# Optimization experiments

Hardware: AMD Instinct MI355X
Metric: run time of the kernel (lower is better)

The kernel has to match this reference:

```python
import jax, jax.numpy as jnp
import numpy as np

N_LAYER = 6
EPS = 1e-5
THETA = 2.0 ** 16


def _ln(x):
    # LayerNorm without affine params, eps=1e-5 (torch default)
    m = x.mean(-1, keepdims=True)
    v = ((x - m) ** 2).mean(-1, keepdims=True)
    return (x - m) * jax.lax.rsqrt(v + EPS)


def _rope(phases, v):
    # rotate-half over interleaved pairs, phases are in cycles (mod 1 -> radians)
    v_rot = jnp.stack([-v[..., 1::2], v[..., ::2]], axis=-1).reshape(v.shape)
    ph = (phases % 1.0) * (2.0 * jnp.pi)
    return v * jnp.cos(ph) + v_rot * jnp.sin(ph)


def _forward(x, conv_w, conv_b, pos_embed, encoder, encoder_v, decoder, freqs, head_w, head_b):
    B, Cin, H, W = x.shape
    nh, D, N = encoder.shape
    P = conv_w.shape[-1]
    hp, wp = H // P, W // P
    T = hp * wp
    # patch embed: Conv2d(k=P, s=P) == unfold + matmul
    xp = x.reshape(B, Cin, hp, P, wp, P)
    tokens = jnp.einsum('bchpwq,dcpq->bhwd', xp, conv_w).reshape(B, T, D) + conv_b
    h = tokens + pos_embed  # (B, T, D); the unit head dim is handled by einsum broadcasting
    phases = jnp.arange(T, dtype=jnp.float32).reshape(1, 1, T, 1) * freqs  # (1,1,T,N)
    scale = 1.0 / jnp.sqrt(jnp.asarray(N, dtype=x.dtype))
    for _ in range(N_LAYER):  # weights are SHARED across layers, as in the module
        hn = _ln(h)  # (B, T, D)
        x_sparse = jax.nn.relu(jnp.einsum('btd,hdn->bhtn', hn, encoder))  # (B,nh,T,N)
        qr = _rope(phases, x_sparse)
        scores = jax.nn.softmax(jnp.einsum('bhtn,bhsn->bhts', qr, qr) * scale, axis=-1)
        yKV = _ln(jnp.einsum('bhts,bsd->bhtd', scores, hn))  # V = ln'd x, broadcast over heads
        y_sparse = jax.nn.relu(jnp.einsum('bhtd,hdn->bhtn', yKV, encoder_v))
        xy_sparse = x_sparse * y_sparse  # (B,nh,T,N)
        z = xy_sparse.transpose(0, 2, 1, 3).reshape(B, T, nh * N)  # (B,T,nh*N), head-major flatten
        yMLP = _ln(z @ decoder)  # (B,T,D)
        h = _ln(hn + yMLP)
    pooled = _ln(h.mean(axis=1))  # (B,D)
    return pooled @ head_w.T + head_b


def setup_inputs():
    key = jax.random.key(0)
    B, Cin, H, P = 64, 3, 224, 16
    D, nh, mult, ncls = 768, 12, 8, 1000
    N = mult * D // nh  # 512
    T = (H // P) ** 2  # 196
    ks = jax.random.split(key, 7)

    def xav(k, shape, fan_in, fan_out):
        a = (6.0 / (fan_in + fan_out)) ** 0.5
        return jax.random.uniform(k, shape, jnp.float32, -a, a)

    x = jax.random.normal(ks[0], (B, Cin, H, H), jnp.float32)
    conv_w = xav(ks[1], (D, Cin, P, P), Cin * P * P, D)
    conv_b = jnp.zeros((D,), jnp.float32)
    pos_embed = jax.random.normal(ks[2], (1, T, D), jnp.float32) * 0.02
    encoder = xav(ks[3], (nh, D, N), D, N)
    encoder_v = xav(ks[4], (nh, D, N), D, N)
    decoder = xav(ks[5], (nh * N, D), nh * N, D)
    i = jnp.arange(N, dtype=jnp.float32)
    freqs = ((1.0 / THETA) ** ((i // 2) * 2.0 / N)).reshape(1, 1, 1, N)  # paired RoPE freqs
    head_w = xav(ks[6], (ncls, D), D, ncls)
    head_b = jnp.zeros((ncls,), jnp.float32)
    return dict(x=x, conv_w=conv_w, conv_b=conv_b, pos_embed=pos_embed,
                encoder=encoder, encoder_v=encoder_v, decoder=decoder,
                freqs=freqs, head_w=head_w, head_b=head_b)


def reference(x, conv_w, conv_b, pos_embed, encoder, encoder_v, decoder, freqs, head_w, head_b):
    return _forward(x, conv_w, conv_b, pos_embed, encoder, encoder_v, decoder, freqs, head_w, head_b)
```

## Files before the change

kernel.cpp:

```cpp
#include <hip/hip_runtime.h>
#include <hip/hip_bf16.h>


typedef short bf16x8 __attribute__((ext_vector_type(8)));
typedef float f32x4 __attribute__((ext_vector_type(4)));
typedef unsigned short u16;

#define LN_EPS 1e-5f
#define SM_SCALE 0.044194173824159216f
#define TWO_PI 6.283185307179586f
#define MC 3136

typedef __attribute__((address_space(3))) unsigned char* as3p;
typedef const __attribute__((address_space(1))) unsigned char* as1p;

__device__ __forceinline__ void gload16(const u16* g, u16* l) {
    __builtin_amdgcn_global_load_lds((as1p)(const void*)g, (as3p)(void*)l, 16, 0, 0);
}

__device__ __forceinline__ u16 f2bf(float f) {
    __hip_bfloat16 h = __float2bfloat16(f);
    return *reinterpret_cast<u16*>(&h);
}
__device__ __forceinline__ float bf2f(u16 u) {
    return __uint_as_float(((unsigned)u) << 16);
}

__device__ __forceinline__ float block_reduce_sum(float v, float* sm) {
    #pragma unroll
    for (int o = 32; o; o >>= 1) v += __shfl_xor(v, o);
    if ((threadIdx.x & 63) == 0) sm[threadIdx.x >> 6] = v;
    __syncthreads();
    float r = sm[0] + sm[1] + sm[2] + sm[3];
    __syncthreads();
    return r;
}

__device__ __forceinline__ void gemm_core64(const u16* __restrict__ A, int lda,
                                            const u16* __restrict__ Bt, int ldb,
                                            int ksteps, f32x4 acc[4][4],
                                            u16* lds_a, u16* lds_b) {
    const int tid = threadIdx.x;
    const int lane = tid & 63;
    const int wave = tid >> 6;
    const int wr = (wave >> 1) * 64;
    const int wc = (wave & 1) * 64;
    const int lr = lane & 15;
    const int lg = lane >> 4;
    const int rx = lr & 7;
    const int srow = tid >> 3;
    const int gslot = (tid & 7) ^ (srow & 7);
    const u16* ga = A + (long)srow * lda + gslot * 8;
    const u16* gb = Bt + (long)srow * ldb + gslot * 8;
    u16* la = lds_a + tid * 8;
    u16* lb = lds_b + tid * 8;
    for (int k0 = 0; k0 < ksteps; ++k0) {
        __syncthreads();
        #pragma unroll
        for (int j = 0; j < 4; ++j) {
            gload16(ga + (long)(j * 32) * lda, la + j * 2048);
            gload16(gb + (long)(j * 32) * ldb, lb + j * 2048);
        }
        ga += 64; gb += 64;
        __syncthreads();
        bf16x8 af[2][4], bfr[2][4];
        #pragma unroll
        for (int kk = 0; kk < 2; ++kk) {
            const int ps = ((lg + kk * 4) ^ rx) * 8;
            #pragma unroll
            for (int m = 0; m < 4; m++)
                af[kk][m] = *(const bf16x8*)&lds_a[(wr + 16 * m + lr) * 64 + ps];
            #pragma unroll
            for (int n = 0; n < 4; n++)
                bfr[kk][n] = *(const bf16x8*)&lds_b[(wc + 16 * n + lr) * 64 + ps];
        }
        #pragma unroll
        for (int kk = 0; kk < 2; ++kk)
            #pragma unroll
            for (int m = 0; m < 4; m++)
                #pragma unroll
                for (int n = 0; n < 4; n++)
                    acc[m][n] = __builtin_amdgcn_mfma_f32_16x16x32_bf16(
                        af[kk][m], bfr[kk][n], acc[m][n], 0, 0, 0);
    }
}

#define GEMM64_PROLOGUE                                 \
    __shared__ alignas(16) u16 lds_ab[2 * 128 * 64];    \
    u16* lds_a = lds_ab;                                \
    u16* lds_b = lds_ab + 128 * 64;                     \
    f32x4 acc[4][4];                                    \
    _Pragma("unroll")                                   \
    for (int m = 0; m < 4; m++)                         \
        _Pragma("unroll")                               \
        for (int n = 0; n < 4; n++)                     \
            acc[m][n] = (f32x4){0.f, 0.f, 0.f, 0.f};

#define EPI_VARS                                        \
    const int lane = threadIdx.x & 63;                  \
    const int wave = threadIdx.x >> 6;                  \
    const int ewr = (wave >> 1) * 64 + (lane >> 4) * 4; \
    const int ewc = (wave & 1) * 64 + (lane & 15);

__global__ __launch_bounds__(256) void k_pack_patches(const float* __restrict__ x,
                                                      u16* __restrict__ ap) {
    int idx = blockIdx.x * 256 + threadIdx.x;
    int r = idx / 768, k = idx - r * 768;
    int b = r / 196, t = r - b * 196;
    int hp = t / 14, wp = t - hp * 14;
    int c = k >> 8, rem = k & 255, p = rem >> 4, q = rem & 15;
    long src = ((long)(b * 3 + c) * 224 + hp * 16 + p) * 224 + wp * 16 + q;
    ap[idx] = f2bf(x[src]);
}

__global__ __launch_bounds__(256) void k_cast(const float* __restrict__ s,
                                              u16* __restrict__ d, int n) {
    int i = blockIdx.x * 256 + threadIdx.x;
    if (i < n) d[i] = f2bf(s[i]);
}

__global__ __launch_bounds__(256) void k_transpose_cast(const float* __restrict__ src,
                                                        u16* __restrict__ dst,
                                                        int R, int C) {
    __shared__ float tile[32][33];
    int c0 = blockIdx.x * 32, r0 = blockIdx.y * 32;
    long base = (long)blockIdx.z * R * C;
    int i = threadIdx.x >> 5, j = threadIdx.x & 31;
    #pragma unroll
    for (int p = 0; p < 4; p++) {
        int rr = i + p * 8;
        tile[rr][j] = src[base + (long)(r0 + rr) * C + c0 + j];
    }
    __syncthreads();
    #pragma unroll
    for (int p = 0; p < 4; p++) {
        int rr = i + p * 8;
        dst[base + (long)(c0 + rr) * R + r0 + j] = f2bf(tile[j][rr]);
    }
}

__global__ __launch_bounds__(256) void k_rope_tab(const float* __restrict__ freqs,
                                                  float* __restrict__ tc,
                                                  float* __restrict__ ts) {
    int idx = blockIdx.x * 256 + threadIdx.x;
    int t = idx >> 9, n = idx & 511;
    float ph = (float)t * freqs[n];
    ph = (ph - floorf(ph)) * TWO_PI;
    tc[idx] = cosf(ph);
    ts[idx] = sinf(ph);
}

__global__ __launch_bounds__(256) void k_colsum(const float* __restrict__ encv,
                                                float* __restrict__ cs) {
    int h = blockIdx.y, c = blockIdx.x * 256 + threadIdx.x;
    const float* base = encv + (long)h * 768 * 512 + c;
    float a = 0.f;
    for (int d = 0; d < 768; d++) a += base[(long)d * 512];
    cs[h * 512 + c] = a;
}

__global__ __launch_bounds__(256) void k_gemm_tokens(const u16* __restrict__ ap,
                                                     const u16* __restrict__ bw,
                                                     const float* __restrict__ cb,
                                                     const float* __restrict__ pe,
                                                     float* __restrict__ hout) {
    GEMM64_PROLOGUE
    int row0 = blockIdx.x * 128, col0 = blockIdx.y * 128;
    gemm_core64(ap + (long)row0 * 768, 768, bw + (long)col0 * 768, 768, 12, acc, lds_a, lds_b);
    EPI_VARS
    const int tid = threadIdx.x;
    float* TF = (float*)lds_ab;
    #pragma unroll
    for (int hf = 0; hf < 2; ++hf) {
        __syncthreads();
        if ((ewr >> 6) == hf) {
            #pragma unroll
            for (int m = 0; m < 4; m++)
                #pragma unroll
                for (int n = 0; n < 4; n++)
                    #pragma unroll
                    for (int i = 0; i < 4; i++) {
                        int row = row0 + ewr + 16 * m + i;
                        int col = col0 + ewc + 16 * n;
                        int t = row % 196;
                        TF[(ewr - hf * 64 + 16 * m + i) * 128 + ewc + 16 * n] =
                            acc[m][n][i] + cb[col] + pe[t * 768 + col];
                    }
        }
        __syncthreads();
        #pragma unroll
        for (int q = 0; q < 8; ++q) {
            int chunk = tid + q * 256;
            int r = chunk >> 5, c = chunk & 31;
            *(f32x4*)&hout[(long)(row0 + hf * 64 + r) * 768 + col0 + c * 4] =
                *(f32x4*)&TF[r * 128 + c * 4];
        }
    }
}

__global__ __launch_bounds__(256) void k_gemm_xs(const u16* __restrict__ hnb,
                                                 const u16* __restrict__ enct,
                                                 const float* __restrict__ tc,
                                                 const float* __restrict__ tsn,
                                                 u16* __restrict__ xs,
                                                 u16* __restrict__ qr) {
    GEMM64_PROLOGUE
    int p = blockIdx.x + 25 * blockIdx.y;
    int w = (p & 7) * 150 + (p >> 3);
    int row0 = (w % 25) * 128, col0 = (w / 25) * 128;
    int head = col0 >> 9, nn0 = col0 & 511;
    gemm_core64(hnb + (long)row0 * 768, 768,
                enct + ((long)head * 512 + nn0) * 768, 768, 12, acc, lds_a, lds_b);
    EPI_VARS
    const int tid = threadIdx.x;
    u16* TU = lds_ab;
    __syncthreads();
    #pragma unroll
    for (int m = 0; m < 4; m++)
        #pragma unroll
        for (int n = 0; n < 4; n++)
            #pragma unroll
            for (int i = 0; i < 4; i++)
                TU[(ewr + 16 * m + i) * 128 + ewc + 16 * n] =
                    f2bf(fmaxf(acc[m][n][i], 0.f));
    __syncthreads();
    #pragma unroll
    for (int q = 0; q < 8; ++q) {
        int chunk = tid + q * 256;
        int r = chunk >> 4, c = chunk & 15;
        int row = row0 + r;
        if (row < MC)
            *(bf16x8*)&xs[((long)head * MC + row) * 512 + nn0 + c * 8] =
                *(bf16x8*)&TU[r * 128 + c * 8];
    }
    #pragma unroll
    for (int q = 0; q < 8; ++q) {
        int chunk = tid + q * 256;
        int r = chunk >> 4, c = chunk & 15;
        int row = row0 + r;
        if (row < MC) {
            int t = row % 196;
            int nn = nn0 + c * 8;
            bf16x8 v8 = *(bf16x8*)&TU[r * 128 + c * 8];
            f32x4 cs0 = *(const f32x4*)&tc[t * 512 + nn];
            f32x4 cs1 = *(const f32x4*)&tc[t * 512 + nn + 4];
            f32x4 sn0 = *(const f32x4*)&tsn[t * 512 + nn];
            f32x4 sn1 = *(const f32x4*)&tsn[t * 512 + nn + 4];
            float v[8], qv[8];
            #pragma unroll
            for (int j = 0; j < 8; j++) v[j] = bf2f((u16)v8[j]);
            #pragma unroll
            for (int j = 0; j < 2; j++) {
                qv[2 * j]     = v[2 * j] * cs0[2 * j]     - v[2 * j + 1] * sn0[2 * j];
                qv[2 * j + 1] = v[2 * j + 1] * cs0[2 * j + 1] + v[2 * j] * sn0[2 * j + 1];
                qv[4 + 2 * j]     = v[4 + 2 * j] * cs1[2 * j]     - v[4 + 2 * j + 1] * sn1[2 * j];
                qv[4 + 2 * j + 1] = v[4 + 2 * j + 1] * cs1[2 * j + 1] + v[4 + 2 * j] * sn1[2 * j + 1];
            }
            bf16x8 o8;
            #pragma unroll
            for (int j = 0; j < 8; j++) o8[j] = (short)f2bf(qv[j]);
            *(bf16x8*)&qr[((long)head * MC + row) * 512 + nn] = o8;
        }
    }
}

__global__ __launch_bounds__(256) void k_attn(const u16* __restrict__ qr,
                                              const u16* __restrict__ hnT,
                                              u16* __restrict__ ykv,
                                              float* __restrict__ stats) {
    __shared__ alignas(16) u16 Pl[128 * 232];
    __shared__ alignas(16) u16 Bl[128 * 64];
    __shared__ float part[2][128][2];
    const int tid = threadIdx.x, lane = tid & 63, wave = tid >> 6;
    const int wr = (wave >> 1) * 64, wc = (wave & 1) * 64;
    const int lr = lane & 15, lg = lane >> 4, lk = lg * 8;
    const int rx = lr & 7;
    const int p = blockIdx.x;
    const int xcd = p & 7, slot = p >> 3;
    const int bL = 2 * xcd + (slot >= 24);
    const int sub = (slot >= 24) ? slot - 24 : slot;
    const int h = sub >> 1, rt = sub & 1;
    const int bh = h * 16 + bL;
    const int row0 = rt * 128;
    const u16* qbase = qr + (long)bh * 196 * 512;

    f32x4 acc0[4][4], acc1[4][4];
    #pragma unroll
    for (int m = 0; m < 4; m++)
        #pragma unroll
        for (int n = 0; n < 4; n++) {
            acc0[m][n] = (f32x4){0.f, 0.f, 0.f, 0.f};
            acc1[m][n] = (f32x4){0.f, 0.f, 0.f, 0.f};
        }
    {
        u16* sA = Pl;
        u16* sB = Pl + 128 * 64;
        gemm_core64(qbase + (long)row0 * 512, 512, qbase, 512, 8, acc0, sA, sB);
        gemm_core64(qbase + (long)row0 * 512, 512, qbase + 128 * 512, 512, 8, acc1, sA, sB);
    }

    const int rb = wr + (lane >> 4) * 4;
    #pragma unroll
    for (int m = 0; m < 4; m++)
        #pragma unroll
        for (int i = 0; i < 4; i++) {
            float mx = -1e30f;
            #pragma unroll
            for (int n = 0; n < 4; n++) {
                int c0 = wc + 16 * n + lr;
                if (c0 < 196) mx = fmaxf(mx, acc0[m][n][i]);
                if (c0 + 128 < 196) mx = fmaxf(mx, acc1[m][n][i]);
            }
            #pragma unroll
            for (int o = 1; o < 16; o <<= 1) mx = fmaxf(mx, __shfl_xor(mx, o));
            if (lr == 0) part[0][rb + 16 * m + i][wave & 1] = mx;
        }
    __syncthreads();
    #pragma unroll
    for (int m = 0; m < 4; m++)
        #pragma unroll
        for (int i = 0; i < 4; i++) {
            int row = rb + 16 * m + i;
            float rmx = fmaxf(part[0][row][0], part[0][row][1]);
            float s = 0.f;
            #pragma unroll
            for (int n = 0; n < 4; n++) {
                int c0 = wc + 16 * n + lr;
                float e0 = (c0 < 196) ? __expf((acc0[m][n][i] - rmx) * SM_SCALE) : 0.f;
                float e1 = (c0 + 128 < 196) ? __expf((acc1[m][n][i] - rmx) * SM_SCALE) : 0.f;
                acc0[m][n][i] = e0; acc1[m][n][i] = e1;
                s += e0 + e1;
            }
            #pragma unroll
            for (int o = 1; o < 16; o <<= 1) s += __shfl_xor(s, o);
            if (lr == 0) part[1][row][wave & 1] = s;
        }
    __syncthreads();
    #pragma unroll
    for (int m = 0; m < 4; m++)
        #pragma unroll
        for (int i = 0; i < 4; i++) {
            int row = rb + 16 * m + i;
            float inv = 1.f / (part[1][row][0] + part[1][row][1]);
            #pragma unroll
            for (int n = 0; n < 4; n++) {
                int c0 = wc + 16 * n + lr;
                Pl[row * 232 + c0] = f2bf(acc0[m][n][i] * inv);
                if (c0 + 128 < 224)
                    Pl[row * 232 + c0 + 128] = f2bf(acc1[m][n][i] * inv);
            }
        }
    __syncthreads();
    { float* pf = &part[0][0][0]; pf[tid] = 0.f; pf[tid + 256] = 0.f; }
    __syncthreads();

    const int srow8 = tid >> 3;
    const int gsl8 = (tid & 7) ^ (srow8 & 7);
    const int srow2 = tid >> 2;
    const int gsl2 = (tid & 3) ^ ((srow2 >> 1) & 3);
    const int ps32 = (lg ^ ((lr >> 1) & 3)) * 8;
    const u16* hbase = hnT + (long)bL * 768 * 224;
    for (int cd = 0; cd < 6; ++cd) {
        const u16* Bt = hbase + (long)(cd * 128) * 224;
        f32x4 pacc[4][4];
        #pragma unroll
        for (int m = 0; m < 4; m++)
            #pragma unroll
            for (int n = 0; n < 4; n++) pacc[m][n] = (f32x4){0.f, 0.f, 0.f, 0.f};
        for (int k0 = 0; k0 < 3; ++k0) {
            __syncthreads();
            #pragma unroll
            for (int j = 0; j < 4; ++j)
                gload16(Bt + (long)(j * 32 + srow8) * 224 + k0 * 64 + gsl8 * 8,
                        Bl + j * 2048 + tid * 8);
            __syncthreads();
            bf16x8 af[2][4], bfr[2][4];
            #pragma unroll
            for (int kk = 0; kk < 2; ++kk) {
                const int ps = ((lg + 4 * kk) ^ rx) * 8;
                #pragma unroll
                for (int m = 0; m < 4; m++)
                    af[kk][m] = *(const bf16x8*)&Pl[(wr + 16 * m + lr) * 232 +
                                                    k0 * 64 + kk * 32 + lk];
                #pragma unroll
                for (int n = 0; n < 4; n++)
                    bfr[kk][n] = *(const bf16x8*)&Bl[(wc + 16 * n + lr) * 64 + ps];
            }
            #pragma unroll
            for (int kk = 0; kk < 2; ++kk)
                #pragma unroll
                for (int m = 0; m < 4; m++)
                    #pragma unroll
                    for (int n = 0; n < 4; n++)
                        pacc[m][n] = __builtin_amdgcn_mfma_f32_16x16x32_bf16(
                            af[kk][m], bfr[kk][n], pacc[m][n], 0, 0, 0);
        }
        {
            __syncthreads();
            gload16(Bt + (long)srow2 * 224 + 192 + gsl2 * 8, Bl + tid * 8);
            gload16(Bt + (long)(srow2 + 64) * 224 + 192 + gsl2 * 8, Bl + 2048 + tid * 8);
            __syncthreads();
            bf16x8 af[4], bfr[4];
            #pragma unroll
            for (int m = 0; m < 4; m++)
                af[m] = *(const bf16x8*)&Pl[(wr + 16 * m + lr) * 232 + 192 + lk];
            #pragma unroll
            for (int n = 0; n < 4; n++)
                bfr[n] = *(const bf16x8*)&Bl[(wc + 16 * n + lr) * 32 + ps32];
            #pragma unroll
            for (int m = 0; m < 4; m++)
                #pragma unroll
                for (int n = 0; n < 4; n++)
                    pacc[m][n] = __builtin_amdgcn_mfma_f32_16x16x32_bf16(
                        af[m], bfr[n], pacc[m][n], 0, 0, 0);
        }
        #pragma unroll
        for (int m = 0; m < 4; m++)
            #pragma unroll
            for (int i = 0; i < 4; i++) {
                float s = pacc[m][0][i] + pacc[m][1][i] + pacc[m][2][i] + pacc[m][3][i];
                float q2 = pacc[m][0][i] * pacc[m][0][i] + pacc[m][1][i] * pacc[m][1][i] +
                           pacc[m][2][i] * pacc[m][2][i] + pacc[m][3][i] * pacc[m][3][i];
                #pragma unroll
                for (int o = 1; o < 16; o <<= 1) {
                    s += __shfl_xor(s, o);
                    q2 += __shfl_xor(q2, o);
                }
                if (lr == 0) {
                    part[0][rb + 16 * m + i][wave & 1] += s;
                    part[1][rb + 16 * m + i][wave & 1] += q2;
                }
            }
        {
            const int ewr = wr + (lane >> 4) * 4;
            const int ewc = wc + lr;
            #pragma unroll
            for (int m = 0; m < 4; m++)
                #pragma unroll
                for (int n = 0; n < 4; n++)
                    #pragma unroll
                    for (int i = 0; i < 4; i++) {
                        int trow = row0 + ewr + 16 * m + i;
                        if (trow < 196)
                            ykv[((long)bh * 196 + trow) * 768 + cd * 128 + ewc + 16 * n] =
                                f2bf(pacc[m][n][i]);
                    }
        }
    }
    __syncthreads();
    if (tid < 128) {
        int trow = row0 + tid;
        if (trow < 196) {
            float s = part[0][tid][0] + part[0][tid][1];
            float q2 = part[1][tid][0] + part[1][tid][1];
            float mu = s * (1.f / 768.f);
            float var = q2 * (1.f / 768.f) - mu * mu;
            float2 st;
            st.x = mu;
            st.y = rsqrtf(var + LN_EPS);
            *(float2*)&stats[((long)bh * 196 + trow) * 2] = st;
        }
    }
}

__global__ __launch_bounds__(256) void k_gemm_ys(const u16* __restrict__ ykv,
                                                 const u16* __restrict__ encvt,
                                                 const u16* __restrict__ xs,
                                                 const float* __restrict__ stats,
                                                 const float* __restrict__ colsum,
                                                 u16* __restrict__ z) {
    GEMM64_PROLOGUE
    int p = blockIdx.x + 25 * (blockIdx.y + 4 * blockIdx.z);
    int w = (p & 7) * 150 + (p >> 3);
    int rt = w % 25, rem = w / 25;
    int ct = rem & 3, h = rem >> 2;
    int row0 = rt * 128, col0 = ct * 128;
    gemm_core64(ykv + ((long)h * MC + row0) * 768, 768,
                encvt + ((long)h * 512 + col0) * 768, 768, 12, acc, lds_a, lds_b);
    EPI_VARS
    const int tid = threadIdx.x;
    u16* TU = lds_ab;
    __syncthreads();
    #pragma unroll
    for (int q = 0; q < 8; ++q) {
        int chunk = tid + q * 256;
        int r = chunk >> 4, c = chunk & 15;
        *(bf16x8*)&TU[r * 128 + c * 8] =
            *(const bf16x8*)&xs[((long)h * MC + row0 + r) * 512 + col0 + c * 8];
    }
    __syncthreads();
    #pragma unroll
    for (int m = 0; m < 4; m++)
        #pragma unroll
        for (int i = 0; i < 4; i++) {
            int rloc = ewr + 16 * m + i;
            int row = row0 + rloc;
            float mu = 0.f, rs = 0.f;
            if (row < MC) {
                float2 st = *(const float2*)&stats[((long)h * MC + row) * 2];
                mu = st.x; rs = st.y;
            }
            #pragma unroll
            for (int n = 0; n < 4; n++) {
                int cloc = ewc + 16 * n;
                float cs = colsum[h * 512 + col0 + cloc];
                float v = (acc[m][n][i] - mu * cs) * rs;
                v = fmaxf(v, 0.f) * bf2f(TU[rloc * 128 + cloc]);
                TU[rloc * 128 + cloc] = f2bf(v);
            }
        }
    __syncthreads();
    #pragma unroll
    for (int q = 0; q < 8; ++q) {
        int chunk = tid + q * 256;
        int r = chunk >> 4, c = chunk & 15;
        int row = row0 + r;
        if (row < MC)
            *(bf16x8*)&z[(long)row * 6144 + h * 512 + col0 + c * 8] =
                *(bf16x8*)&TU[r * 128 + c * 8];
    }
}

__global__ __launch_bounds__(256) void k_gemm_mlp(const u16* __restrict__ z,
                                                  const u16* __restrict__ dect,
                                                  float* __restrict__ rawK) {
    GEMM64_PROLOGUE
    int p = blockIdx.x + 25 * (blockIdx.y + 6 * blockIdx.z);
    int w = (p & 7) * 75 + (p >> 3);
    int row0 = (w % 25) * 128, col0 = ((w / 25) % 6) * 128, s = w / 150;
    gemm_core64(z + (long)row0 * 6144 + s * 1536, 6144,
                dect + (long)col0 * 6144 + s * 1536, 6144, 24, acc, lds_a, lds_b);
    EPI_VARS
    const int tid = threadIdx.x;
    float* TF = (float*)lds_ab;
    float* raw = rawK + (long)s * MC * 768;
    #pragma unroll
    for (int hf = 0; hf < 2; ++hf) {
        __syncthreads();
        if ((ewr >> 6) == hf) {
            #pragma unroll
            for (int m = 0; m < 4; m++)
                #pragma unroll
                for (int n = 0; n < 4; n++)
                    #pragma unroll
                    for (int i = 0; i < 4; i++)
                        TF[(ewr - hf * 64 + 16 * m + i) * 128 + ewc + 16 * n] =
                            acc[m][n][i];
        }
        __syncthreads();
        #pragma unroll
        for (int q = 0; q < 8; ++q) {
            int chunk = tid + q * 256;
            int r = chunk >> 5, c = chunk & 31;
            int row = row0 + hf * 64 + r;
            if (row < MC)
                *(f32x4*)&raw[(long)row * 768 + col0 + c * 4] =
                    *(f32x4*)&TF[r * 128 + c * 4];
        }
    }
}

__global__ __launch_bounds__(256) void k_ln1(const float* __restrict__ h,
                                             u16* __restrict__ hnb) {
    __shared__ float sm[4];
    int r = blockIdx.x, tid = threadIdx.x;
    const float* p = h + (long)r * 768;
    float x0 = p[tid], x1 = p[tid + 256], x2 = p[tid + 512];
    float mean = block_reduce_sum(x0 + x1 + x2, sm) * (1.f / 768.f);
    float d0 = x0 - mean, d1 = x1 - mean, d2 = x2 - mean;
    float var = block_reduce_sum(d0 * d0 + d1 * d1 + d2 * d2, sm) * (1.f / 768.f);
    float rs = rsqrtf(var + LN_EPS);
    long ro = (long)r * 768;
    hnb[ro + tid] = f2bf(d0 * rs);
    hnb[ro + tid + 256] = f2bf(d1 * rs);
    hnb[ro + tid + 512] = f2bf(d2 * rs);
}

__global__ __launch_bounds__(256) void k_hnT(const u16* __restrict__ hnb,
                                             u16* __restrict__ hnT) {
    __shared__ u16 tile[32][33];
    int t0 = blockIdx.x * 32, d0 = blockIdx.y * 32, b = blockIdx.z;
    int i = threadIdx.x >> 5, j = threadIdx.x & 31;
    #pragma unroll
    for (int p = 0; p < 4; p++) {
        int t = t0 + i + p * 8;
        tile[i + p * 8][j] = (t < 196) ? hnb[((long)b * 196 + t) * 768 + d0 + j] : (u16)0;
    }
    __syncthreads();
    #pragma unroll
    for (int p = 0; p < 4; p++) {
        int dd = i + p * 8;
        hnT[((long)b * 768 + d0 + dd) * 224 + t0 + j] = tile[j][dd];
    }
}

__global__ __launch_bounds__(256) void k_final_h(const float* __restrict__ rawK,
                                                 u16* __restrict__ hnb) {
    __shared__ float sm[4];
    const long PS = (long)MC * 768;
    int r = blockIdx.x, tid = threadIdx.x;
    const float* rp = rawK + (long)r * 768;
    u16* hp = hnb + (long)r * 768;
    float y0 = rp[tid] + rp[tid + PS] + rp[tid + 2 * PS] + rp[tid + 3 * PS];
    float y1 = rp[tid + 256] + rp[tid + 256 + PS] + rp[tid + 256 + 2 * PS] + rp[tid + 256 + 3 * PS];
    float y2 = rp[tid + 512] + rp[tid + 512 + PS] + rp[tid + 512 + 2 * PS] + rp[tid + 512 + 3 * PS];
    float h0 = bf2f(hp[tid]), h1 = bf2f(hp[tid + 256]), h2 = bf2f(hp[tid + 512]);
    float mean = block_reduce_sum(y0 + y1 + y2, sm) * (1.f / 768.f);
    float d0 = y0 - mean, d1 = y1 - mean, d2 = y2 - mean;
    float var = block_reduce_sum(d0 * d0 + d1 * d1 + d2 * d2, sm) * (1.f / 768.f);
    float rs = rsqrtf(var + LN_EPS);
    float s0 = h0 + d0 * rs;
    float s1 = h1 + d1 * rs;
    float s2 = h2 + d2 * rs;
    mean = block_reduce_sum(s0 + s1 + s2, sm) * (1.f / 768.f);
    d0 = s0 - mean; d1 = s1 - mean; d2 = s2 - mean;
    var = block_reduce_sum(d0 * d0 + d1 * d1 + d2 * d2, sm) * (1.f / 768.f);
    rs = rsqrtf(var + LN_EPS);
    hp[tid] = f2bf(d0 * rs);
    hp[tid + 256] = f2bf(d1 * rs);
    hp[tid + 512] = f2bf(d2 * rs);
}

__global__ __launch_bounds__(256) void k_pool1(const u16* __restrict__ hnb,
                                               float* __restrict__ part) {
    int g = blockIdx.x, b = blockIdx.y, tid = threadIdx.x;
    const u16* base = hnb + ((long)b * 196 + g * 14) * 768;
    float a0 = 0.f, a1 = 0.f, a2 = 0.f;
    for (int t = 0; t < 14; t++) {
        const u16* p = base + (long)t * 768;
        a0 += bf2f(p[tid]); a1 += bf2f(p[tid + 256]); a2 += bf2f(p[tid + 512]);
    }
    float* pp = part + ((long)b * 14 + g) * 768;
    pp[tid] = a0; pp[tid + 256] = a1; pp[tid + 512] = a2;
}

__global__ __launch_bounds__(256) void k_pool2(const float* __restrict__ part,
                                               float* __restrict__ pooled) {
    __shared__ float sm[4];
    int b = blockIdx.x, tid = threadIdx.x;
    const float* pp = part + (long)b * 14 * 768;
    float a0 = 0.f, a1 = 0.f, a2 = 0.f;
    for (int g = 0; g < 14; g++) {
        a0 += pp[g * 768 + tid]; a1 += pp[g * 768 + tid + 256]; a2 += pp[g * 768 + tid + 512];
    }
    a0 *= (1.f / 196.f); a1 *= (1.f / 196.f); a2 *= (1.f / 196.f);
    float mean = block_reduce_sum(a0 + a1 + a2, sm) * (1.f / 768.f);
    float d0 = a0 - mean, d1 = a1 - mean, d2 = a2 - mean;
    float var = block_reduce_sum(d0 * d0 + d1 * d1 + d2 * d2, sm) * (1.f / 768.f);
    float rs = rsqrtf(var + LN_EPS);
    pooled[(long)b * 768 + tid] = d0 * rs;
    pooled[(long)b * 768 + tid + 256] = d1 * rs;
    pooled[(long)b * 768 + tid + 512] = d2 * rs;
}

__global__ __launch_bounds__(256) void k_head(const float* __restrict__ pooled,
                                              const float* __restrict__ hw,
                                              const float* __restrict__ hb,
                                              float* __restrict__ out) {
    __shared__ float pr[768];
    int b = blockIdx.y, tid = threadIdx.x;
    pr[tid] = pooled[(long)b * 768 + tid];
    pr[tid + 256] = pooled[(long)b * 768 + tid + 256];
    pr[tid + 512] = pooled[(long)b * 768 + tid + 512];
    __syncthreads();
    int c = blockIdx.x * 4 + (tid >> 6);
    int lane = tid & 63;
    const float* wrow = hw + (long)c * 768;
    float acc = 0.f;
    #pragma unroll
    for (int k = 0; k < 768; k += 64) acc += pr[k + lane] * wrow[k + lane];
    #pragma unroll
    for (int o = 32; o; o >>= 1) acc += __shfl_xor(acc, o);
    if (lane == 0) out[(long)b * 1000 + c] = acc + hb[c];
}

extern "C" void kernel_launch(void* const* d_in, const int* in_sizes, int n_in,
                              void* d_out, int out_size, void* d_ws, size_t ws_size,
                              hipStream_t stream) {
    const float* x     = (const float*)d_in[0];
    const float* convw = (const float*)d_in[1];
    const float* convb = (const float*)d_in[2];
    const float* pe    = (const float*)d_in[3];
    const float* enc   = (const float*)d_in[4];
    const float* encv  = (const float*)d_in[5];
    const float* dec   = (const float*)d_in[6];
    const float* freqs = (const float*)d_in[7];
    const float* hw    = (const float*)d_in[8];
    const float* hbias = (const float*)d_in[9];
    float* out = (float*)d_out;

    char* W = (char*)d_ws;
    size_t off = 0;
    auto ALLOC = [&](size_t bytes) {
        size_t o = off;
        off += (bytes + 255) & ~(size_t)255;
        return o;
    };
    float* bh    = (float*)(W + ALLOC(38535168));
    u16*   bhnb  = (u16*)  (W + ALLOC(19267584 + 524288));
    u16*   bhnT  = (u16*)  (W + ALLOC(22020096));
    u16*   benc  = (u16*)  (W + ALLOC(9437184));
    u16*   bencv = (u16*)  (W + ALLOC(9437184));
    u16*   bdec  = (u16*)  (W + ALLOC(9437184));
    float* btc   = (float*)(W + ALLOC(401408));
    float* bts   = (float*)(W + ALLOC(401408));
    float* bpool = (float*)(W + ALLOC(196608));
    float* bpart = (float*)(W + ALLOC(2752512));
    float* bstats= (float*)(W + ALLOC(301056));
    float* bcs   = (float*)(W + ALLOC(24576));
    char*  R1    = (char*) (W + ALLOC(38535168 + 2097152));
    char*  R2    = (char*) (W + ALLOC(57802752 + 524288));
    char*  R3    = (char*) (W + ALLOC(38535168 + 524288));
    (void)ws_size; (void)in_sizes; (void)n_in; (void)out_size;

    u16*   bap  = (u16*)R2;
    u16*   bcw  = (u16*)R3;
    u16*   qr   = (u16*)R1;
    u16*   z    = (u16*)R1;
    u16*   ykv  = (u16*)R2;
    float* rawK = (float*)R2;
    u16*   xs   = (u16*)R3;

    k_pack_patches<<<37632, 256, 0, stream>>>(x, bap);
    k_cast<<<2304, 256, 0, stream>>>(convw, bcw, 768 * 768);
    k_gemm_tokens<<<dim3(98, 6), 256, 0, stream>>>(bap, bcw, convb, pe, bh);
    k_transpose_cast<<<dim3(16, 24, 12), 256, 0, stream>>>(enc, benc, 768, 512);
    k_transpose_cast<<<dim3(16, 24, 12), 256, 0, stream>>>(encv, bencv, 768, 512);
    k_transpose_cast<<<dim3(24, 192, 1), 256, 0, stream>>>(dec, bdec, 6144, 768);
    k_rope_tab<<<392, 256, 0, stream>>>(freqs, btc, bts);
    k_colsum<<<dim3(2, 12), 256, 0, stream>>>(encv, bcs);
    k_ln1<<<12544, 256, 0, stream>>>(bh, bhnb);

    for (int L = 0; L < 6; ++L) {
        k_hnT<<<dim3(7, 24, 64), 256, 0, stream>>>(bhnb, bhnT);
        for (int c = 0; c < 4; ++c) {
            long r0 = (long)c * MC;
            k_gemm_xs<<<dim3(25, 48), 256, 0, stream>>>(
                bhnb + r0 * 768, benc, btc, bts, xs, qr);
            k_attn<<<384, 256, 0, stream>>>(
                qr, bhnT + (long)c * 16 * 768 * 224, ykv, bstats);
            k_gemm_ys<<<dim3(25, 4, 12), 256, 0, stream>>>(ykv, bencv, xs, bstats, bcs, z);
            k_gemm_mlp<<<dim3(25, 6, 4), 256, 0, stream>>>(z, bdec, rawK);
            k_final_h<<<MC, 256, 0, stream>>>(rawK, bhnb + r0 * 768);
        }
    }

    k_pool1<<<dim3(14, 64), 256, 0, stream>>>(bhnb, bpart);
    k_pool2<<<64, 256, 0, stream>>>(bpart, bpool);
    k_head<<<dim3(250, 64), 256, 0, stream>>>(bpool, hw, hbias, out);
}
```

Before: 5.914 ms.

## Split attention kernel into score/softmax and PV kernels via global probabilities

The fused attention kernel is split in two. The first computes QK^T and softmax and writes bf16 probabilities to a global scratch buffer, reusing the bh buffer, through a smaller LDS staging area. The second streams those probabilities back with global_load_lds tiles alongside hnT for the PV GEMM and LayerNorm stats. This cuts LDS use per kernel (no 128x232 P tile kept resident), which may allow more blocks per CU. The cost is an extra launch and a global round trip for P, and reusing bh as scratch assumes it is dead at that point.

```diff
diff --git a/kernel.cpp b/kernel.cpp
--- a/kernel.cpp
+++ b/kernel.cpp
@@ -102,6 +102,15 @@
     const int ewr = (wave >> 1) * 64 + (lane >> 4) * 4; \
     const int ewc = (wave & 1) * 64 + (lane & 15);
 
+#define ATTN_REMAP                                      \
+    const int p = blockIdx.x;                           \
+    const int xcd = p & 7, slot = p >> 3;               \
+    const int bL = 2 * xcd + (slot >= 24);              \
+    const int sub = (slot >= 24) ? slot - 24 : slot;    \
+    const int h = sub >> 1, rt = sub & 1;               \
+    const int bh = h * 16 + bL;                         \
+    const int row0 = rt * 128;
+
 __global__ __launch_bounds__(256) void k_pack_patches(const float* __restrict__ x,
                                                       u16* __restrict__ ap) {
     int idx = blockIdx.x * 256 + threadIdx.x;
@@ -264,24 +273,14 @@
     }
 }
 
-__global__ __launch_bounds__(256) void k_attn(const u16* __restrict__ qr,
-                                              const u16* __restrict__ hnT,
-                                              u16* __restrict__ ykv,
-                                              float* __restrict__ stats) {
-    __shared__ alignas(16) u16 Pl[128 * 232];
-    __shared__ alignas(16) u16 Bl[128 * 64];
+__global__ __launch_bounds__(256) void k_attn1(const u16* __restrict__ qr,
+                                               u16* __restrict__ Pg) {
+    __shared__ alignas(16) u16 sAB[2 * 128 * 64];
     __shared__ float part[2][128][2];
     const int tid = threadIdx.x, lane = tid & 63, wave = tid >> 6;
     const int wr = (wave >> 1) * 64, wc = (wave & 1) * 64;
-    const int lr = lane & 15, lg = lane >> 4, lk = lg * 8;
-    const int rx = lr & 7;
-    const int p = blockIdx.x;
-    const int xcd = p & 7, slot = p >> 3;
-    const int bL = 2 * xcd + (slot >= 24);
-    const int sub = (slot >= 24) ? slot - 24 : slot;
-    const int h = sub >> 1, rt = sub & 1;
-    const int bh = h * 16 + bL;
-    const int row0 = rt * 128;
+    const int lr = lane & 15;
+    ATTN_REMAP
     const u16* qbase = qr + (long)bh * 196 * 512;
 
     f32x4 acc0[4][4], acc1[4][4];
@@ -292,12 +291,10 @@
             acc0[m][n] = (f32x4){0.f, 0.f, 0.f, 0.f};
             acc1[m][n] = (f32x4){0.f, 0.f, 0.f, 0.f};
         }
-    {
-        u16* sA = Pl;
-        u16* sB = Pl + 128 * 64;
-        gemm_core64(qbase + (long)row0 * 512, 512, qbase, 512, 8, acc0, sA, sB);
-        gemm_core64(qbase + (long)row0 * 512, 512, qbase + 128 * 512, 512, 8, acc1, sA, sB);
-    }
+    gemm_core64(qbase + (long)row0 * 512, 512, qbase, 512, 8, acc0,
+                sAB, sAB + 128 * 64);
+    gemm_core64(qbase + (long)row0 * 512, 512, qbase + 128 * 512, 512, 8, acc1,
+                sAB, sAB + 128 * 64);
 
     const int rb = wr + (lane >> 4) * 4;
     #pragma unroll
@@ -336,30 +333,63 @@
             if (lr == 0) part[1][row][wave & 1] = s;
         }
     __syncthreads();
-    #pragma unroll
-    for (int m = 0; m < 4; m++)
-        #pragma unroll
-        for (int i = 0; i < 4; i++) {
-            int row = rb + 16 * m + i;
-            float inv = 1.f / (part[1][row][0] + part[1][row][1]);
-            #pragma unroll
-            for (int n = 0; n < 4; n++) {
-                int c0 = wc + 16 * n + lr;
-                Pl[row * 232 + c0] = f2bf(acc0[m][n][i] * inv);
-                if (c0 + 128 < 224)
-                    Pl[row * 232 + c0 + 128] = f2bf(acc1[m][n][i] * inv);
-            }
-        }
-    __syncthreads();
-    { float* pf = &part[0][0][0]; pf[tid] = 0.f; pf[tid + 256] = 0.f; }
-    __syncthreads();
-
+    u16* BB = sAB;
+    u16* pt = Pg + (long)(bh * 2 + rt) * 128 * 224;
+    #pragma unroll
+    for (int hf = 0; hf < 2; ++hf) {
+        __syncthreads();
+        if ((wr >> 6) == hf) {
+            #pragma unroll
+            for (int m = 0; m < 4; m++)
+                #pragma unroll
+                for (int i = 0; i < 4; i++) {
+                    int row = rb + 16 * m + i;
+                    int lrow = row - hf * 64;
+                    float inv = 1.f / (part[1][row][0] + part[1][row][1]);
+                    #pragma unroll
+                    for (int n = 0; n < 4; n++) {
+                        int c0 = wc + 16 * n + lr;
+                        BB[lrow * 224 + c0] = f2bf(acc0[m][n][i] * inv);
+                        if (c0 + 128 < 224)
+                            BB[lrow * 224 + c0 + 128] = f2bf(acc1[m][n][i] * inv);
+                    }
+                }
+        }
+        __syncthreads();
+        #pragma unroll
+        for (int q = 0; q < 7; ++q) {
+            int chunk = tid + q * 256;
+            int r = chunk / 28, c = chunk - r * 28;
+            *(bf16x8*)&pt[(long)(hf * 64 + r) * 224 + c * 8] =
+                *(bf16x8*)&BB[r * 224 + c * 8];
+        }
+    }
+}
+
+__global__ __launch_bounds__(256) void k_attn2(const u16* __restrict__ Pg,
+                                               const u16* __restrict__ hnT,
+                                               u16* __restrict__ ykv,
+                                               float* __restrict__ stats) {
+    __shared__ alignas(16) u16 Al[128 * 64];
+    __shared__ alignas(16) u16 Bl[128 * 64];
+    __shared__ float part[2][128][2];
+    const int tid = threadIdx.x, lane = tid & 63, wave = tid >> 6;
+    const int wr = (wave >> 1) * 64, wc = (wave & 1) * 64;
+    const int lr = lane & 15, lg = lane >> 4, lk = lg * 8;
+    const int rx = lr & 7;
+    ATTN_REMAP
+    const int rb = wr + (lane >> 4) * 4;
+    const u16* Pt = Pg + (long)(bh * 2 + rt) * 128 * 224;
+    const u16* hbase = hnT + (long)bL * 768 * 224;
     const int srow8 = tid >> 3;
     const int gsl8 = (tid & 7) ^ (srow8 & 7);
     const int srow2 = tid >> 2;
     const int gsl2 = (tid & 3) ^ ((srow2 >> 1) & 3);
     const int ps32 = (lg ^ ((lr >> 1) & 3)) * 8;
-    const u16* hbase = hnT + (long)bL * 768 * 224;
+
+    { float* pf = &part[0][0][0]; pf[tid] = 0.f; pf[tid + 256] = 0.f; }
+    __syncthreads();
+
     for (int cd = 0; cd < 6; ++cd) {
         const u16* Bt = hbase + (long)(cd * 128) * 224;
         f32x4 pacc[4][4];
@@ -370,9 +400,12 @@
         for (int k0 = 0; k0 < 3; ++k0) {
             __syncthreads();
             #pragma unroll
-            for (int j = 0; j < 4; ++j)
+            for (int j = 0; j < 4; ++j) {
+                gload16(Pt + (long)(j * 32 + srow8) * 224 + k0 * 64 + gsl8 * 8,
+                        Al + j * 2048 + tid * 8);
                 gload16(Bt + (long)(j * 32 + srow8) * 224 + k0 * 64 + gsl8 * 8,
                         Bl + j * 2048 + tid * 8);
+            }
             __syncthreads();
             bf16x8 af[2][4], bfr[2][4];
             #pragma unroll
@@ -380,8 +413,7 @@
                 const int ps = ((lg + 4 * kk) ^ rx) * 8;
                 #pragma unroll
                 for (int m = 0; m < 4; m++)
-                    af[kk][m] = *(const bf16x8*)&Pl[(wr + 16 * m + lr) * 232 +
-                                                    k0 * 64 + kk * 32 + lk];
+                    af[kk][m] = *(const bf16x8*)&Al[(wr + 16 * m + lr) * 64 + ps];
                 #pragma unroll
                 for (int n = 0; n < 4; n++)
                     bfr[kk][n] = *(const bf16x8*)&Bl[(wc + 16 * n + lr) * 64 + ps];
@@ -397,13 +429,15 @@
         }
         {
             __syncthreads();
+            gload16(Pt + (long)srow2 * 224 + 192 + gsl2 * 8, Al + tid * 8);
+            gload16(Pt + (long)(srow2 + 64) * 224 + 192 + gsl2 * 8, Al + 2048 + tid * 8);
             gload16(Bt + (long)srow2 * 224 + 192 + gsl2 * 8, Bl + tid * 8);
             gload16(Bt + (long)(srow2 + 64) * 224 + 192 + gsl2 * 8, Bl + 2048 + tid * 8);
             __syncthreads();
             bf16x8 af[4], bfr[4];
             #pragma unroll
             for (int m = 0; m < 4; m++)
-                af[m] = *(const bf16x8*)&Pl[(wr + 16 * m + lr) * 232 + 192 + lk];
+                af[m] = *(const bf16x8*)&Al[(wr + 16 * m + lr) * 32 + ps32];
             #pragma unroll
             for (int n = 0; n < 4; n++)
                 bfr[n] = *(const bf16x8*)&Bl[(wc + 16 * n + lr) * 32 + ps32];
@@ -720,6 +754,7 @@
     u16*   ykv  = (u16*)R2;
     float* rawK = (float*)R2;
     u16*   xs   = (u16*)R3;
+    u16*   Pg   = (u16*)bh;
 
     k_pack_patches<<<37632, 256, 0, stream>>>(x, bap);
     k_cast<<<2304, 256, 0, stream>>>(convw, bcw, 768 * 768);
@@ -737,8 +772,9 @@
             long r0 = (long)c * MC;
             k_gemm_xs<<<dim3(25, 48), 256, 0, stream>>>(
                 bhnb + r0 * 768, benc, btc, bts, xs, qr);
-            k_attn<<<384, 256, 0, stream>>>(
-                qr, bhnT + (long)c * 16 * 768 * 224, ykv, bstats);
+            k_attn1<<<384, 256, 0, stream>>>(qr, Pg);
+            k_attn2<<<384, 256, 0, stream>>>(
+                Pg, bhnT + (long)c * 16 * 768 * 224, ykv, bstats);
             k_gemm_ys<<<dim3(25, 4, 12), 256, 0, stream>>>(ykv, bencv, xs, bstats, bcs, z);
             k_gemm_mlp<<<dim3(25, 6, 4), 256, 0, stream>>>(z, bdec, rawK);
             k_final_h<<<MC, 256, 0, stream>>>(rawK, bhnb + r0 * 768);
```

Result: slower. 6.348 ms (+7.3%).
